# Optimization experiments

Hardware: AMD Instinct MI355X
Metric: run time of the kernel (lower is better)

The kernel has to match this reference:

```python
import math
import jax, jax.numpy as jnp
import numpy as np

L, C, FC, K, H, WIN, T, B = 6, 512, 2048, 3, 8, 4, 1024, 4
KC = C // H
EPS = 1e-4


def setup_inputs() -> dict:
    key = jax.random.key(0)
    ks = jax.random.split(key, 20)
    s = 0.05
    f = jnp.float32
    inp = {
        "x": jax.random.normal(ks[0], (B, C, T), f),
        "wq": jax.random.normal(ks[1], (L, C, C), f) * s,
        "bq": jnp.zeros((L, C), f),
        "wk": jax.random.normal(ks[2], (L, C, C), f) * s,
        "bk": jnp.zeros((L, C), f),
        "wv": jax.random.normal(ks[3], (L, C, C), f) * s,
        "bv": jnp.zeros((L, C), f),
        "wo": jax.random.normal(ks[4], (L, C, C), f) * s,
        "bo": jnp.zeros((L, C), f),
        "rel_k": jax.random.normal(ks[5], (L, 1, 2 * WIN + 1, KC), f) * (KC ** -0.5),
        "g1": jnp.ones((L, C), f),
        "be1": jnp.zeros((L, C), f),
        "w1": jax.random.normal(ks[6], (L, FC, C, K), f) * s,
        "bb1": jnp.zeros((L, FC), f),
        "w2": jax.random.normal(ks[7], (L, C, FC, K), f) * s,
        "bb2": jnp.zeros((L, C), f),
        "g2": jnp.ones((L, C), f),
        "be2": jnp.zeros((L, C), f),
    }
    return inp


def conv1d(x, w, b, pad):
    # x: [B,Cin,T], w: [Cout,Cin,K]
    y = jax.lax.conv_general_dilated(x, w, (1,), [(pad, pad)],
                                     dimension_numbers=("NCH", "OIH", "NCH"))
    return y + b[None, :, None]


def layer_norm(x, g, b):
    # normalize over channel dim (axis 1), matching the torch LayerNorm above
    m = jnp.mean(x, 1, keepdims=True)
    v = jnp.mean((x - m) ** 2, 1, keepdims=True)
    return (x - m) * jax.lax.rsqrt(v + EPS) * g[None, :, None] + b[None, :, None]


def get_relative_embeddings(rel, length):
    pad_len = max(length - (WIN + 1), 0)
    start = max(WIN + 1 - length, 0)
    if pad_len > 0:
        rel = jnp.pad(rel, ((0, 0), (pad_len, pad_len), (0, 0)), mode="edge")
    return rel[:, start:start + 2 * length - 1]


def rel_to_abs(x):
    # x: [b,h,l,2l-1] -> [b,h,l,l]  (Music-Transformer skew)
    b, h, l, _ = x.shape
    x = jnp.pad(x, ((0, 0), (0, 0), (0, 0), (0, 1)))          # [b,h,l,2l]
    x = x.reshape(b, h, l * 2 * l)
    x = jnp.pad(x, ((0, 0), (0, 0), (0, l - 1)))
    x = x.reshape(b, h, l + 1, 2 * l - 1)[:, :, :l, l - 1:]
    return x


def attention(x, wq, bq, wk, bk, wv, bv, wo, bo, rel_k):
    b, c, t = x.shape
    q = conv1d(x, wq[:, :, None], bq, 0).reshape(b, H, KC, t)
    k = conv1d(x, wk[:, :, None], bk, 0).reshape(b, H, KC, t)
    v = conv1d(x, wv[:, :, None], bv, 0).reshape(b, H, KC, t)
    scale = 1.0 / math.sqrt(KC)
    scores = jnp.einsum("bhdt,bhds->bhts", q, k) * scale      # [b,H,t,t]
    rel = get_relative_embeddings(rel_k, t)[0]                # [2t-1, KC] (heads_share)
    rel_logits = jnp.einsum("bhdt,md->bhtm", q * scale, rel)  # [b,H,t,2t-1]
    scores = scores + rel_to_abs(rel_logits)
    p = jax.nn.softmax(scores, axis=-1)
    out = jnp.einsum("bhts,bhds->bhdt", p, v).reshape(b, c, t)
    return conv1d(out, wo[:, :, None], bo, 0)


def reference(x, wq, bq, wk, bk, wv, bv, wo, bo, rel_k,
              g1, be1, w1, bb1, w2, bb2, g2, be2):
    for i in range(L):
        y = attention(x, wq[i], bq[i], wk[i], bk[i], wv[i], bv[i],
                      wo[i], bo[i], rel_k[i])
        x = layer_norm(x + y, g1[i], be1[i])
        y = conv1d(jax.nn.relu(conv1d(x, w1[i], bb1[i], K // 2)), w2[i], bb2[i], K // 2)
        x = layer_norm(x + y, g2[i], be2[i])
    return x
```

## Files before the change

### kernel.cpp

```cpp
#include <hip/hip_runtime.h>

constexpr int L  = 6;
constexpr int C  = 512;
constexpr int FC = 2048;
constexpr int H  = 8;
constexpr int KC = 64;
constexpr int T  = 1024;
constexpr int B  = 4;
#define SCALE 0.125f
#define LOG2E 1.4426950408889634f

typedef __bf16 bf16_t;
typedef __bf16 bf16x8 __attribute__((ext_vector_type(8)));
typedef float  f32x4  __attribute__((ext_vector_type(4)));

constexpr size_t OFF_XF    = 0;
constexpr size_t OFF_YF    = OFF_XF   + (size_t)B*T*C*4;
constexpr size_t OFF_XPAD  = OFF_YF   + (size_t)B*T*C*4;
constexpr size_t OFF_Q     = OFF_XPAD + (size_t)B*(T+2)*C*2;
constexpr size_t OFF_K     = OFF_Q    + (size_t)B*T*C*2;
constexpr size_t OFF_VT    = OFF_K    + (size_t)B*T*C*2;
constexpr size_t OFF_YA    = OFF_VT   + (size_t)B*T*C*2;
constexpr size_t OFF_MID   = OFF_YA   + (size_t)B*T*C*2;
constexpr size_t OFF_WQKVO = OFF_MID  + (size_t)B*(T+2)*FC*2;
constexpr size_t OFF_W1    = OFF_WQKVO+ (size_t)4*C*C*2;
constexpr size_t OFF_W2    = OFF_W1   + (size_t)3*FC*C*2;

__device__ __forceinline__ void gload_lds16(const bf16_t* g, bf16_t* l) {
    __builtin_amdgcn_global_load_lds((const __attribute__((address_space(1))) void*)g,
                                     (__attribute__((address_space(3))) void*)l, 16, 0, 0);
}

__global__ __launch_bounds__(256) void cvt4_kernel(const float* __restrict__ a,
                                                   const float* __restrict__ b,
                                                   const float* __restrict__ c,
                                                   const float* __restrict__ d,
                                                   bf16_t* __restrict__ out) {
    int i = blockIdx.x * 256 + threadIdx.x;
    int which = i >> 18;
    int idx   = i & ((1 << 18) - 1);
    const float* s = (which == 0) ? a : (which == 1) ? b : (which == 2) ? c : d;
    out[i] = (bf16_t)s[idx];
}

__global__ __launch_bounds__(256) void cvtw1_kernel(const float* __restrict__ w1, bf16_t* __restrict__ out) {
    int i = blockIdx.x * 256 + threadIdx.x;
    int j = i >> 20;
    int rem = i & ((1 << 20) - 1);
    int fc = rem >> 9, c = rem & 511;
    out[i] = (bf16_t)w1[fc * (C * 3) + c * 3 + j];
}

__global__ __launch_bounds__(256) void cvtw2_kernel(const float* __restrict__ w2, bf16_t* __restrict__ out) {
    int i = blockIdx.x * 256 + threadIdx.x;
    int j = i >> 20;
    int rem = i & ((1 << 20) - 1);
    int c = rem >> 11, fc = rem & 2047;
    out[i] = (bf16_t)w2[c * (FC * 3) + fc * 3 + j];
}

__global__ __launch_bounds__(256) void transpose_in(const float* __restrict__ x0,
                                                    float* __restrict__ xf,
                                                    bf16_t* __restrict__ xpad) {
    __shared__ float tile[32][33];
    int b = blockIdx.z, t0 = blockIdx.x * 32, c0 = blockIdx.y * 32;
    int tx = threadIdx.x, ty = threadIdx.y;
#pragma unroll
    for (int j = 0; j < 4; ++j)
        tile[ty + j * 8][tx] = x0[((size_t)b * C + c0 + ty + j * 8) * T + t0 + tx];
    __syncthreads();
#pragma unroll
    for (int j = 0; j < 4; ++j) {
        float v = tile[tx][ty + j * 8];
        long t = t0 + ty + j * 8;
        xf[((size_t)b * T + t) * C + c0 + tx] = v;
        xpad[((size_t)b * (T + 2) + t + 1) * C + c0 + tx] = (bf16_t)v;
    }
}

__global__ __launch_bounds__(256) void transpose_out(const float* __restrict__ xf,
                                                     float* __restrict__ out) {
    __shared__ float tile[32][33];
    int b = blockIdx.z, t0 = blockIdx.x * 32, c0 = blockIdx.y * 32;
    int tx = threadIdx.x, ty = threadIdx.y;
#pragma unroll
    for (int j = 0; j < 4; ++j)
        tile[ty + j * 8][tx] = xf[((size_t)b * T + t0 + ty + j * 8) * C + c0 + tx];
    __syncthreads();
#pragma unroll
    for (int j = 0; j < 4; ++j)
        out[((size_t)b * C + c0 + ty + j * 8) * T + t0 + tx] = tile[tx][ty + j * 8];
}

__global__ __launch_bounds__(256) void zero_pads(bf16_t* __restrict__ xpad, bf16_t* __restrict__ midp) {
    int i = blockIdx.x * 256 + threadIdx.x;
    if (i < 4096) {
        int b = i >> 10, r = (i >> 9) & 1, c = i & 511;
        xpad[((size_t)b * (T + 2) + (size_t)r * (T + 1)) * C + c] = (bf16_t)0.f;
    } else {
        int j = i - 4096;
        int b = j >> 12, r = (j >> 11) & 1, c = j & 2047;
        midp[((size_t)b * (T + 2) + (size_t)r * (T + 1)) * FC + c] = (bf16_t)0.f;
    }
}

template <int NP>
__global__ __launch_bounds__(256) void add_ln(float* __restrict__ x,
                                              const float* __restrict__ p0, const float* __restrict__ p1,
                                              const float* __restrict__ p2,
                                              const float* __restrict__ g, const float* __restrict__ be,
                                              bf16_t* __restrict__ xpad) {
    long bt = blockIdx.x;
    int tid = threadIdx.x;
    float* xr = x + bt * C;
    float v0 = xr[tid] + p0[bt * C + tid] + p1[bt * C + tid];
    float v1 = xr[tid + 256] + p0[bt * C + tid + 256] + p1[bt * C + tid + 256];
    if (NP == 3) { v0 += p2[bt * C + tid]; v1 += p2[bt * C + tid + 256]; }
    float s = v0 + v1, q = v0 * v0 + v1 * v1;
#pragma unroll
    for (int m = 1; m < 64; m <<= 1) { s += __shfl_xor(s, m); q += __shfl_xor(q, m); }
    __shared__ float ss[4], qq[4];
    int wid = tid >> 6;
    if ((tid & 63) == 0) { ss[wid] = s; qq[wid] = q; }
    __syncthreads();
    s = ss[0] + ss[1] + ss[2] + ss[3];
    q = qq[0] + qq[1] + qq[2] + qq[3];
    float mean = s * (1.f / C);
    float var = q * (1.f / C) - mean * mean;
    float rstd = rsqrtf(var + 1e-4f);
    float o0 = (v0 - mean) * rstd * g[tid] + be[tid];
    float o1 = (v1 - mean) * rstd * g[tid + 256] + be[tid + 256];
    xr[tid] = o0; xr[tid + 256] = o1;
    long b = bt >> 10, t = bt & (T - 1);
    bf16_t* xp = xpad + (b * (T + 2) + t + 1) * C;
    xp[tid] = (bf16_t)o0; xp[tid + 256] = (bf16_t)o1;
}

template <int OUTMODE, bool RELU, int NSPLIT, int IPT, int NTAPS>
__global__ __launch_bounds__(256) void gemm128(
    const bf16_t* __restrict__ A, long batchStrideA, int lda,
    const bf16_t* __restrict__ Bw, long tapStrideB, int ldb,
    const float* __restrict__ bias0, const float* __restrict__ bias1,
    const float* __restrict__ bias2,
    void* __restrict__ Dp, void* __restrict__ D1p, void* __restrict__ D2p,
    long batchStrideD, int ldd) {
    __shared__ bf16_t As[128 * 64];
    __shared__ bf16_t Bs[128 * 64];
    const int tid = threadIdx.x;
    const int lane = tid & 63, wid = tid >> 6;
    const int l15 = lane & 15, quad = lane >> 4;
    const int wy = wid >> 1, wx = wid & 1;
    const int nb = gridDim.z / NSPLIT;
    const int split = (NSPLIT > 1) ? ((int)blockIdx.z / nb) : 0;
    const int b = (int)blockIdx.z - split * nb;

    const bf16_t* Ab = A + (long)b * batchStrideA + (long)blockIdx.y * 128 * lda;
    const bf16_t* Bb = Bw + (long)blockIdx.x * 128 * ldb;

    const int lrow = lane >> 3;
    const int lcolsw = ((lane & 7) ^ lrow) * 8;

    f32x4 acc[4][4];
#pragma unroll
    for (int i = 0; i < 4; ++i)
#pragma unroll
        for (int j = 0; j < 4; ++j) acc[i][j] = (f32x4){0.f, 0.f, 0.f, 0.f};

    constexpr int itersAll = IPT * NTAPS;
    constexpr int per = itersAll / NSPLIT;
    const int it0 = split * per;

    for (int it = it0; it < it0 + per; ++it) {
        const int tap = (NTAPS == 1) ? 0 : (it / IPT);
        const int k0 = (it - tap * IPT) * 64;
        const bf16_t* At = Ab + (long)tap * lda + k0;
        const bf16_t* Bt = Bb + (long)tap * tapStrideB + k0;
        __syncthreads();
#pragma unroll
        for (int i = 0; i < 4; ++i) {
            int chunk = wid * 4 + i;
            int row = chunk * 8 + lrow;
            gload_lds16(At + (long)row * lda + lcolsw, As + chunk * 512 + lane * 8);
            gload_lds16(Bt + (long)row * ldb + lcolsw, Bs + chunk * 512 + lane * 8);
        }
        __syncthreads();
#pragma unroll
        for (int ks = 0; ks < 2; ++ks) {
            bf16x8 bfr[4], afr[4];
#pragma unroll
            for (int nt = 0; nt < 4; ++nt) {
                int row = wx * 64 + nt * 16 + l15;
                bfr[nt] = *(const bf16x8*)&Bs[row * 64 + (((ks * 4 + quad) ^ (l15 & 7)) * 8)];
            }
#pragma unroll
            for (int mt = 0; mt < 4; ++mt) {
                int row = wy * 64 + mt * 16 + l15;
                afr[mt] = *(const bf16x8*)&As[row * 64 + (((ks * 4 + quad) ^ (l15 & 7)) * 8)];
            }
#pragma unroll
            for (int mt = 0; mt < 4; ++mt)
#pragma unroll
                for (int nt = 0; nt < 4; ++nt)
                    acc[mt][nt] = __builtin_amdgcn_mfma_f32_16x16x32_bf16(afr[mt], bfr[nt], acc[mt][nt], 0, 0, 0);
        }
    }

    const long m0 = (long)blockIdx.y * 128 + wy * 64;
    const int n0g = (int)blockIdx.x * 128 + wx * 64;
#pragma unroll
    for (int mt = 0; mt < 4; ++mt) {
        long rowb = m0 + mt * 16 + quad * 4;
#pragma unroll
        for (int nt = 0; nt < 4; ++nt) {
            int col = n0g + nt * 16 + l15;
            if (OUTMODE == 0) {
                float bb = (split == 0) ? bias0[col] : 0.f;
                float* D = ((split == 0) ? (float*)Dp : (split == 1) ? (float*)D1p : (float*)D2p)
                           + (long)b * batchStrideD;
#pragma unroll
                for (int r = 0; r < 4; ++r) D[(rowb + r) * ldd + col] = acc[mt][nt][r] + bb;
            } else if (OUTMODE == 1) {
                float bb = bias0[col];
                bf16_t* D = (bf16_t*)Dp + (long)b * batchStrideD;
#pragma unroll
                for (int r = 0; r < 4; ++r) {
                    float v = acc[mt][nt][r] + bb;
                    if (RELU) v = fmaxf(v, 0.f);
                    D[(rowb + r) * ldd + col] = (bf16_t)v;
                }
            } else {
                int which = col >> 9, cl = col & 511;
                const float* bp = (which == 0) ? bias0 : (which == 1) ? bias1 : bias2;
                float bb = bp[cl];
                if (which < 2) {
                    bf16_t* D = (bf16_t*)((which == 0) ? Dp : D1p) + (long)b * T * C;
#pragma unroll
                    for (int r = 0; r < 4; ++r) D[(rowb + r) * C + cl] = (bf16_t)(acc[mt][nt][r] + bb);
                } else {
                    bf16_t* D = (bf16_t*)D2p + (long)b * C * T;
                    union { bf16_t h[4]; uint2 u; } pk;
#pragma unroll
                    for (int r = 0; r < 4; ++r) pk.h[r] = (bf16_t)(acc[mt][nt][r] + bb);
                    *(uint2*)(D + (long)cl * T + rowb) = pk.u;
                }
            }
        }
    }
}

__global__ __launch_bounds__(256) void attn_kernel(const bf16_t* __restrict__ q,
                                                   const bf16_t* __restrict__ k,
                                                   const bf16_t* __restrict__ vT,
                                                   const float* __restrict__ relk,
                                                   bf16_t* __restrict__ y) {
    const int b = blockIdx.z, h = blockIdx.y;
    const int qt0 = blockIdx.x * 64;
    __shared__ bf16_t qps[64 * 72];
    __shared__ bf16_t ktb[2][64 * 64];
    __shared__ bf16_t vtb[2][64 * 64];
    __shared__ float  rl[64][12];

    const int tid = threadIdx.x;
    const int lane = tid & 63, wid = tid >> 6;
    const int l15 = lane & 15, quad = lane >> 4;
    const int lrow = lane >> 3;
    const int su   = ((lane & 7) ^ lrow) * 8;

    const bf16_t* qbase = q + ((size_t)(b * T + qt0)) * C + h * 64;
    const bf16_t* kbs = k + ((size_t)(b * T)) * C + h * 64;
    const bf16_t* vbs = vT + ((size_t)(b * C + h * 64)) * T;

#pragma unroll
    for (int i = 0; i < 2; ++i) {
        int chunk = wid * 2 + i;
        int row = chunk * 8 + lrow;
        gload_lds16(qbase + (long)row * C + su, qps + chunk * 512 + lane * 8);
        gload_lds16(kbs + (long)row * C + su, ktb[0] + chunk * 512 + lane * 8);
        gload_lds16(vbs + (long)row * T + su, vtb[0] + chunk * 512 + lane * 8);
    }
    __syncthreads();

    for (int i = tid; i < 64 * 9; i += 256) {
        int r = i / 9, j = i - r * 9;
        float acc = 0.f;
#pragma unroll
        for (int d = 0; d < 64; ++d)
            acc += (float)qps[r * 64 + ((d >> 3) ^ (r & 7)) * 8 + (d & 7)] * relk[j * 64 + d];
        rl[r][j] = acc * (SCALE * LOG2E);
    }
    __syncthreads();

    const int qrow = wid * 16 + l15;
    bf16x8 af[2];
#pragma unroll
    for (int ks = 0; ks < 2; ++ks)
        af[ks] = *(const bf16x8*)&qps[qrow * 64 + (((ks * 4 + quad) ^ (qrow & 7)) * 8)];
    const float rl0 = rl[qrow][0], rl8 = rl[qrow][8];

    float m_i = -1e30f, l_i = 0.f;
    f32x4 o[4];
#pragma unroll
    for (int dn = 0; dn < 4; ++dn) o[dn] = (f32x4){0.f, 0.f, 0.f, 0.f};

    bf16_t* myP = qps + wid * (16 * 72);

    for (int st = 0; st < T / 64; ++st) {
        __syncthreads();
        if (st < T / 64 - 1) {
            const bf16_t* kb2 = kbs + (size_t)(st + 1) * 64 * C;
            const bf16_t* vb2 = vbs + (st + 1) * 64;
            bf16_t* kd = ktb[(st + 1) & 1];
            bf16_t* vd = vtb[(st + 1) & 1];
#pragma unroll
            for (int i = 0; i < 2; ++i) {
                int chunk = wid * 2 + i, row = chunk * 8 + lrow;
                gload_lds16(kb2 + (long)row * C + su, kd + chunk * 512 + lane * 8);
                gload_lds16(vb2 + (long)row * T + su, vd + chunk * 512 + lane * 8);
            }
        }
        const bf16_t* ktc = ktb[st & 1];
        const bf16_t* vtc = vtb[st & 1];

        f32x4 sc[4];
#pragma unroll
        for (int nt = 0; nt < 4; ++nt) {
            f32x4 a = (f32x4){0.f, 0.f, 0.f, 0.f};
#pragma unroll
            for (int ks = 0; ks < 2; ++ks) {
                int rr = nt * 16 + l15;
                bf16x8 kfr = *(const bf16x8*)&ktc[rr * 64 + (((ks * 4 + quad) ^ (l15 & 7)) * 8)];
                a = __builtin_amdgcn_mfma_f32_16x16x32_bf16(kfr, af[ks], a, 0, 0, 0);
            }
            sc[nt] = a;
        }

        const int base = st * 64 - qt0 - wid * 16;
        if (base >= 32) {
#pragma unroll
            for (int nt = 0; nt < 4; ++nt)
#pragma unroll
                for (int r = 0; r < 4; ++r) sc[nt][r] = sc[nt][r] * (SCALE * LOG2E) + rl8;
        } else if (base <= -80) {
#pragma unroll
            for (int nt = 0; nt < 4; ++nt)
#pragma unroll
                for (int r = 0; r < 4; ++r) sc[nt][r] = sc[nt][r] * (SCALE * LOG2E) + rl0;
        } else {
#pragma unroll
            for (int nt = 0; nt < 4; ++nt)
#pragma unroll
                for (int r = 0; r < 4; ++r) {
                    int j = base + nt * 16 + quad * 4 + r - l15 + 4;
                    j = j < 0 ? 0 : (j > 8 ? 8 : j);
                    sc[nt][r] = sc[nt][r] * (SCALE * LOG2E) + rl[qrow][j];
                }
        }

        float mx = fmaxf(fmaxf(fmaxf(sc[0][0], sc[0][1]), fmaxf(sc[0][2], sc[0][3])),
                         fmaxf(fmaxf(sc[1][0], sc[1][1]), fmaxf(sc[1][2], sc[1][3])));
        mx = fmaxf(mx, fmaxf(fmaxf(fmaxf(sc[2][0], sc[2][1]), fmaxf(sc[2][2], sc[2][3])),
                             fmaxf(fmaxf(sc[3][0], sc[3][1]), fmaxf(sc[3][2], sc[3][3]))));
        mx = fmaxf(mx, __shfl_xor(mx, 16));
        mx = fmaxf(mx, __shfl_xor(mx, 32));
        float mn = fmaxf(m_i, mx);
        float alpha = exp2f(m_i - mn);
        m_i = mn;
        float rs = 0.f;
#pragma unroll
        for (int nt = 0; nt < 4; ++nt)
#pragma unroll
            for (int r = 0; r < 4; ++r) {
                float p = exp2f(sc[nt][r] - m_i);
                sc[nt][r] = p;
                rs += p;
            }
        rs += __shfl_xor(rs, 16);
        rs += __shfl_xor(rs, 32);
        l_i = l_i * alpha + rs;
#pragma unroll
        for (int dn = 0; dn < 4; ++dn) o[dn] *= alpha;

#pragma unroll
        for (int nt = 0; nt < 4; ++nt) {
            union { bf16_t hh[4]; uint2 u; } pk;
#pragma unroll
            for (int r = 0; r < 4; ++r) pk.hh[r] = (bf16_t)sc[nt][r];
            *(uint2*)&myP[l15 * 72 + nt * 16 + quad * 4] = pk.u;
        }

        bf16x8 pb[2];
#pragma unroll
        for (int ks = 0; ks < 2; ++ks)
            pb[ks] = *(const bf16x8*)&myP[l15 * 72 + ks * 32 + quad * 8];
#pragma unroll
        for (int dn = 0; dn < 4; ++dn)
#pragma unroll
            for (int ks = 0; ks < 2; ++ks) {
                int rr = dn * 16 + l15;
                bf16x8 vf = *(const bf16x8*)&vtc[rr * 64 + (((ks * 4 + quad) ^ (l15 & 7)) * 8)];
                o[dn] = __builtin_amdgcn_mfma_f32_16x16x32_bf16(vf, pb[ks], o[dn], 0, 0, 0);
            }
    }

    float linv = 1.f / l_i;
    bf16_t* yb = y + ((size_t)(b * T + qt0 + qrow)) * C + h * 64;
#pragma unroll
    for (int dn = 0; dn < 4; ++dn) {
        union { bf16_t hh[4]; uint2 u; } pk;
#pragma unroll
        for (int r = 0; r < 4; ++r) pk.hh[r] = (bf16_t)(o[dn][r] * linv);
        *(uint2*)(yb + dn * 16 + quad * 4) = pk.u;
    }
}

extern "C" void kernel_launch(void* const* d_in, const int* in_sizes, int n_in,
                              void* d_out, int out_size, void* d_ws, size_t ws_size,
                              hipStream_t stream) {
    const float* x0  = (const float*)d_in[0];
    const float* wq  = (const float*)d_in[1];
    const float* bq  = (const float*)d_in[2];
    const float* wk  = (const float*)d_in[3];
    const float* bk  = (const float*)d_in[4];
    const float* wv  = (const float*)d_in[5];
    const float* bv  = (const float*)d_in[6];
    const float* wo  = (const float*)d_in[7];
    const float* bo  = (const float*)d_in[8];
    const float* rlk = (const float*)d_in[9];
    const float* g1  = (const float*)d_in[10];
    const float* be1 = (const float*)d_in[11];
    const float* w1  = (const float*)d_in[12];
    const float* bb1 = (const float*)d_in[13];
    const float* w2  = (const float*)d_in[14];
    const float* bb2 = (const float*)d_in[15];
    const float* g2  = (const float*)d_in[16];
    const float* be2 = (const float*)d_in[17];

    char* ws = (char*)d_ws;
    float*  xf    = (float*)(ws + OFF_XF);
    float*  yf    = (float*)(ws + OFF_YF);
    float*  yf2   = (float*)(ws + OFF_Q);
    float*  yf3   = (float*)(ws + OFF_VT);
    bf16_t* xpad  = (bf16_t*)(ws + OFF_XPAD);
    bf16_t* qb    = (bf16_t*)(ws + OFF_Q);
    bf16_t* kb    = (bf16_t*)(ws + OFF_K);
    bf16_t* vTb   = (bf16_t*)(ws + OFF_VT);
    bf16_t* yab   = (bf16_t*)(ws + OFF_YA);
    bf16_t* midp  = (bf16_t*)(ws + OFF_MID);
    bf16_t* wqkvo = (bf16_t*)(ws + OFF_WQKVO);
    bf16_t* w1b   = (bf16_t*)(ws + OFF_W1);
    bf16_t* w2b   = (bf16_t*)(ws + OFF_W2);

    transpose_in<<<dim3(T / 32, C / 32, B), dim3(32, 8), 0, stream>>>(x0, xf, xpad);
    zero_pads<<<80, 256, 0, stream>>>(xpad, midp);

    for (int l = 0; l < L; ++l) {
        cvt4_kernel<<<4 * C * C / 256, 256, 0, stream>>>(wq + (size_t)l * C * C, wk + (size_t)l * C * C,
                                                         wv + (size_t)l * C * C, wo + (size_t)l * C * C, wqkvo);
        cvtw1_kernel<<<3 * FC * C / 256, 256, 0, stream>>>(w1 + (size_t)l * FC * C * 3, w1b);
        cvtw2_kernel<<<3 * C * FC / 256, 256, 0, stream>>>(w2 + (size_t)l * C * FC * 3, w2b);

        gemm128<3, false, 1, 8, 1><<<dim3(1536 / 128, T / 128, B), 256, 0, stream>>>(
            xpad + C, (long)(T + 2) * C, C, wqkvo, 0, C,
            bq + l * C, bk + l * C, bv + l * C,
            (void*)qb, (void*)kb, (void*)vTb, 0, 0);

        attn_kernel<<<dim3(T / 64, H, B), 256, 0, stream>>>(qb, kb, vTb, rlk + (size_t)l * 9 * KC, yab);

        gemm128<0, false, 2, 8, 1><<<dim3(C / 128, T / 128, 2 * B), 256, 0, stream>>>(
            yab, (long)T * C, C, wqkvo + 3 * C * C, 0, C,
            bo + l * C, nullptr, nullptr,
            (void*)yf, (void*)yf2, nullptr, (long)T * C, C);

        add_ln<2><<<B * T, 256, 0, stream>>>(xf, yf, yf2, nullptr, g1 + l * C, be1 + l * C, xpad);

        gemm128<1, true, 1, 8, 3><<<dim3(FC / 128, T / 128, B), 256, 0, stream>>>(
            xpad, (long)(T + 2) * C, C, w1b, (long)FC * C, C,
            bb1 + l * FC, nullptr, nullptr,
            (void*)(midp + FC), nullptr, nullptr, (long)(T + 2) * FC, FC);

        gemm128<0, false, 3, 32, 3><<<dim3(C / 128, T / 128, 3 * B), 256, 0, stream>>>(
            midp, (long)(T + 2) * FC, FC, w2b, (long)C * FC, FC,
            bb2 + l * C, nullptr, nullptr,
            (void*)yf, (void*)yf2, (void*)yf3, (long)T * C, C);

        add_ln<3><<<B * T, 256, 0, stream>>>(xf, yf, yf2, yf3, g2 + l * C, be2 + l * C, xpad);
    }

    transpose_out<<<dim3(T / 32, C / 32, B), dim3(32, 8), 0, stream>>>(xf, (float*)d_out);
}
```

Measured before the change: 1.239 ms.

## Add narrow 128x64 GEMM tile variant and merge weight conversion kernels

Makes the GEMM's N-tile width a template parameter. A 64-wide variant uses four waves stacked along M, and it is applied to the QKV, output-projection and second FFN GEMMs. This doubles the block count so more of the GPU's compute units are filled on these small grids, at the cost of less B-operand reuse per tile. The three per-layer weight conversion kernels are also merged into one launch to cut launch overhead.

```diff
diff --git a/kernel.cpp b/kernel.cpp
--- a/kernel.cpp
+++ b/kernel.cpp
@@ -31,32 +31,36 @@
                                      (__attribute__((address_space(3))) void*)l, 16, 0, 0);
 }
 
-__global__ __launch_bounds__(256) void cvt4_kernel(const float* __restrict__ a,
-                                                   const float* __restrict__ b,
-                                                   const float* __restrict__ c,
-                                                   const float* __restrict__ d,
-                                                   bf16_t* __restrict__ out) {
+__global__ __launch_bounds__(256) void cvt_all(const float* __restrict__ a,
+                                               const float* __restrict__ bq_,
+                                               const float* __restrict__ c,
+                                               const float* __restrict__ d,
+                                               const float* __restrict__ w1,
+                                               const float* __restrict__ w2,
+                                               bf16_t* __restrict__ wqkvo,
+                                               bf16_t* __restrict__ w1b,
+                                               bf16_t* __restrict__ w2b) {
     int i = blockIdx.x * 256 + threadIdx.x;
-    int which = i >> 18;
-    int idx   = i & ((1 << 18) - 1);
-    const float* s = (which == 0) ? a : (which == 1) ? b : (which == 2) ? c : d;
-    out[i] = (bf16_t)s[idx];
-}
-
-__global__ __launch_bounds__(256) void cvtw1_kernel(const float* __restrict__ w1, bf16_t* __restrict__ out) {
-    int i = blockIdx.x * 256 + threadIdx.x;
-    int j = i >> 20;
-    int rem = i & ((1 << 20) - 1);
-    int fc = rem >> 9, c = rem & 511;
-    out[i] = (bf16_t)w1[fc * (C * 3) + c * 3 + j];
-}
-
-__global__ __launch_bounds__(256) void cvtw2_kernel(const float* __restrict__ w2, bf16_t* __restrict__ out) {
-    int i = blockIdx.x * 256 + threadIdx.x;
-    int j = i >> 20;
-    int rem = i & ((1 << 20) - 1);
-    int c = rem >> 11, fc = rem & 2047;
-    out[i] = (bf16_t)w2[c * (FC * 3) + fc * 3 + j];
+    constexpr int N4 = 4 * C * C;
+    constexpr int NW1 = 3 * FC * C;
+    if (i < N4) {
+        int which = i >> 18;
+        int idx   = i & ((1 << 18) - 1);
+        const float* s = (which == 0) ? a : (which == 1) ? bq_ : (which == 2) ? c : d;
+        wqkvo[i] = (bf16_t)s[idx];
+    } else if (i < N4 + NW1) {
+        int t = i - N4;
+        int j = t >> 20;
+        int rem = t & ((1 << 20) - 1);
+        int fc = rem >> 9, cc = rem & 511;
+        w1b[t] = (bf16_t)w1[fc * (C * 3) + cc * 3 + j];
+    } else {
+        int t = i - N4 - NW1;
+        int j = t >> 20;
+        int rem = t & ((1 << 20) - 1);
+        int cc = rem >> 11, fc = rem & 2047;
+        w2b[t] = (bf16_t)w2[cc * (FC * 3) + fc * 3 + j];
+    }
 }
 
 __global__ __launch_bounds__(256) void transpose_in(const float* __restrict__ x0,
@@ -136,7 +140,7 @@
     xp[tid] = (bf16_t)o0; xp[tid + 256] = (bf16_t)o1;
 }
 
-template <int OUTMODE, bool RELU, int NSPLIT, int IPT, int NTAPS>
+template <int OUTMODE, bool RELU, int NSPLIT, int IPT, int NTAPS, int BNT>
 __global__ __launch_bounds__(256) void gemm128(
     const bf16_t* __restrict__ A, long batchStrideA, int lda,
     const bf16_t* __restrict__ Bw, long tapStrideB, int ldb,
@@ -145,24 +149,29 @@
     void* __restrict__ Dp, void* __restrict__ D1p, void* __restrict__ D2p,
     long batchStrideD, int ldd) {
     __shared__ bf16_t As[128 * 64];
-    __shared__ bf16_t Bs[128 * 64];
+    __shared__ bf16_t Bs[BNT * 64];
+    constexpr int WAVES_Y = (BNT == 128) ? 2 : 4;
+    constexpr int WM = 128 / WAVES_Y;
+    constexpr int MT = WM / 16;
+    constexpr int CPW = BNT / 32;
     const int tid = threadIdx.x;
     const int lane = tid & 63, wid = tid >> 6;
     const int l15 = lane & 15, quad = lane >> 4;
-    const int wy = wid >> 1, wx = wid & 1;
+    const int wy = (BNT == 128) ? (wid >> 1) : wid;
+    const int wx = (BNT == 128) ? (wid & 1) : 0;
     const int nb = gridDim.z / NSPLIT;
     const int split = (NSPLIT > 1) ? ((int)blockIdx.z / nb) : 0;
     const int b = (int)blockIdx.z - split * nb;
 
     const bf16_t* Ab = A + (long)b * batchStrideA + (long)blockIdx.y * 128 * lda;
-    const bf16_t* Bb = Bw + (long)blockIdx.x * 128 * ldb;
+    const bf16_t* Bb = Bw + (long)blockIdx.x * BNT * ldb;
 
     const int lrow = lane >> 3;
     const int lcolsw = ((lane & 7) ^ lrow) * 8;
 
-    f32x4 acc[4][4];
-#pragma unroll
-    for (int i = 0; i < 4; ++i)
+    f32x4 acc[MT][4];
+#pragma unroll
+    for (int i = 0; i < MT; ++i)
 #pragma unroll
         for (int j = 0; j < 4; ++j) acc[i][j] = (f32x4){0.f, 0.f, 0.f, 0.f};
 
@@ -181,34 +190,39 @@
             int chunk = wid * 4 + i;
             int row = chunk * 8 + lrow;
             gload_lds16(At + (long)row * lda + lcolsw, As + chunk * 512 + lane * 8);
+        }
+#pragma unroll
+        for (int i = 0; i < CPW; ++i) {
+            int chunk = wid * CPW + i;
+            int row = chunk * 8 + lrow;
             gload_lds16(Bt + (long)row * ldb + lcolsw, Bs + chunk * 512 + lane * 8);
         }
         __syncthreads();
 #pragma unroll
         for (int ks = 0; ks < 2; ++ks) {
-            bf16x8 bfr[4], afr[4];
+            bf16x8 bfr[4], afr[MT];
 #pragma unroll
             for (int nt = 0; nt < 4; ++nt) {
                 int row = wx * 64 + nt * 16 + l15;
                 bfr[nt] = *(const bf16x8*)&Bs[row * 64 + (((ks * 4 + quad) ^ (l15 & 7)) * 8)];
             }
 #pragma unroll
-            for (int mt = 0; mt < 4; ++mt) {
-                int row = wy * 64 + mt * 16 + l15;
+            for (int mt = 0; mt < MT; ++mt) {
+                int row = wy * WM + mt * 16 + l15;
                 afr[mt] = *(const bf16x8*)&As[row * 64 + (((ks * 4 + quad) ^ (l15 & 7)) * 8)];
             }
 #pragma unroll
-            for (int mt = 0; mt < 4; ++mt)
+            for (int mt = 0; mt < MT; ++mt)
 #pragma unroll
                 for (int nt = 0; nt < 4; ++nt)
                     acc[mt][nt] = __builtin_amdgcn_mfma_f32_16x16x32_bf16(afr[mt], bfr[nt], acc[mt][nt], 0, 0, 0);
         }
     }
 
-    const long m0 = (long)blockIdx.y * 128 + wy * 64;
-    const int n0g = (int)blockIdx.x * 128 + wx * 64;
-#pragma unroll
-    for (int mt = 0; mt < 4; ++mt) {
+    const long m0 = (long)blockIdx.y * 128 + wy * WM;
+    const int n0g = (int)blockIdx.x * BNT + wx * 64;
+#pragma unroll
+    for (int mt = 0; mt < MT; ++mt) {
         long rowb = m0 + mt * 16 + quad * 4;
 #pragma unroll
         for (int nt = 0; nt < 4; ++nt) {
@@ -453,32 +467,34 @@
     transpose_in<<<dim3(T / 32, C / 32, B), dim3(32, 8), 0, stream>>>(x0, xf, xpad);
     zero_pads<<<80, 256, 0, stream>>>(xpad, midp);
 
+    constexpr int CVT_BLOCKS = (4 * C * C + 3 * FC * C + 3 * C * FC) / 256;
+
     for (int l = 0; l < L; ++l) {
-        cvt4_kernel<<<4 * C * C / 256, 256, 0, stream>>>(wq + (size_t)l * C * C, wk + (size_t)l * C * C,
-                                                         wv + (size_t)l * C * C, wo + (size_t)l * C * C, wqkvo);
-        cvtw1_kernel<<<3 * FC * C / 256, 256, 0, stream>>>(w1 + (size_t)l * FC * C * 3, w1b);
-        cvtw2_kernel<<<3 * C * FC / 256, 256, 0, stream>>>(w2 + (size_t)l * C * FC * 3, w2b);
-
-        gemm128<3, false, 1, 8, 1><<<dim3(1536 / 128, T / 128, B), 256, 0, stream>>>(
+        cvt_all<<<CVT_BLOCKS, 256, 0, stream>>>(wq + (size_t)l * C * C, wk + (size_t)l * C * C,
+                                                wv + (size_t)l * C * C, wo + (size_t)l * C * C,
+                                                w1 + (size_t)l * FC * C * 3, w2 + (size_t)l * C * FC * 3,
+                                                wqkvo, w1b, w2b);
+
+        gemm128<3, false, 1, 8, 1, 64><<<dim3(1536 / 64, T / 128, B), 256, 0, stream>>>(
             xpad + C, (long)(T + 2) * C, C, wqkvo, 0, C,
             bq + l * C, bk + l * C, bv + l * C,
             (void*)qb, (void*)kb, (void*)vTb, 0, 0);
 
         attn_kernel<<<dim3(T / 64, H, B), 256, 0, stream>>>(qb, kb, vTb, rlk + (size_t)l * 9 * KC, yab);
 
-        gemm128<0, false, 2, 8, 1><<<dim3(C / 128, T / 128, 2 * B), 256, 0, stream>>>(
+        gemm128<0, false, 2, 8, 1, 64><<<dim3(C / 64, T / 128, 2 * B), 256, 0, stream>>>(
             yab, (long)T * C, C, wqkvo + 3 * C * C, 0, C,
             bo + l * C, nullptr, nullptr,
             (void*)yf, (void*)yf2, nullptr, (long)T * C, C);
 
         add_ln<2><<<B * T, 256, 0, stream>>>(xf, yf, yf2, nullptr, g1 + l * C, be1 + l * C, xpad);
 
-        gemm128<1, true, 1, 8, 3><<<dim3(FC / 128, T / 128, B), 256, 0, stream>>>(
+        gemm128<1, true, 1, 8, 3, 128><<<dim3(FC / 128, T / 128, B), 256, 0, stream>>>(
             xpad, (long)(T + 2) * C, C, w1b, (long)FC * C, C,
             bb1 + l * FC, nullptr, nullptr,
             (void*)(midp + FC), nullptr, nullptr, (long)(T + 2) * FC, FC);
 
-        gemm128<0, false, 3, 32, 3><<<dim3(C / 128, T / 128, 3 * B), 256, 0, stream>>>(
+        gemm128<0, false, 3, 32, 3, 64><<<dim3(C / 64, T / 128, 3 * B), 256, 0, stream>>>(
             midp, (long)(T + 2) * FC, FC, w2b, (long)C * FC, FC,
             bb2 + l * C, nullptr, nullptr,
             (void*)yf, (void*)yf2, (void*)yf3, (long)T * C, C);
```

New measurement: 1.156 ms. 6.7% less time.
